# Performance work log

Hardware: AMD Instinct MI355X
Metric: run time of the kernel (lower is better)

Reference implementation:

```python
import jax, jax.numpy as jnp
import numpy as np
from jax import lax

B, CIN, L = 2048, 1024, 30
E, C = 8, 2            # num_experts, num_classes
FC_IN = 256 * 9        # 2304
FIN_IN = C + 512 * L + 256 * (L // 2 + 1)  # 19458


def _maxpool1d(x):
    # MaxPool1d(kernel=2, stride=2, padding=1); pad with -inf like torch
    return lax.reduce_window(x, -jnp.inf, lax.max,
                             (1, 1, 2), (1, 1, 2),
                             [(0, 0), (0, 0), (1, 1)])


def _conv1d(x, w):
    # x: [B,Cin,L], w: [Cout,Cin,3], padding=1
    return lax.conv_general_dilated(x, w, (1,), [(1, 1)],
                                    dimension_numbers=('NCH', 'OIH', 'NCH'))


def setup_inputs() -> dict:
    key = jax.random.key(0)
    ks = jax.random.split(key, 16)
    s = 0.02
    inp = {
        'x': jax.random.normal(ks[0], (B, CIN, L), jnp.float32),
        'expert_idx': jax.random.randint(ks[1], (B,), 0, E),
        'conv1_w': jax.random.normal(ks[2], (512, 1024, 3), jnp.float32) * s,
        'conv1_b': jnp.zeros((512,), jnp.float32),
        'conv2_w': jax.random.normal(ks[3], (256, 512, 3), jnp.float32) * s,
        'conv2_b': jnp.zeros((256,), jnp.float32),
        'fc_w': jax.random.normal(ks[4], (1024, FC_IN), jnp.float32) * s,
        'fc_b': jnp.zeros((1024,), jnp.float32),
        'e_w1': jax.random.normal(ks[5], (E, 512, 1024), jnp.float32) * s,
        'e_b1': jnp.zeros((E, 512), jnp.float32),
        'e_w2': jax.random.normal(ks[6], (E, C, 512), jnp.float32) * s,
        'e_b2': jnp.zeros((E, C), jnp.float32),
        'agg_w': jax.random.normal(ks[7], (C, E * C), jnp.float32) * s,
        'agg_b': jnp.zeros((C,), jnp.float32),
        'fin_w': jax.random.normal(ks[8], (C, FIN_IN), jnp.float32) * s,
        'fin_b': jnp.zeros((C,), jnp.float32),
    }
    return inp


def reference(x, expert_idx, conv1_w, conv1_b, conv2_w, conv2_b, fc_w, fc_b,
              e_w1, e_b1, e_w2, e_b2, agg_w, agg_b, fin_w, fin_b):
    b = x.shape[0]
    # shared feature extractor
    x1 = jax.nn.relu(_conv1d(x, conv1_w) + conv1_b[None, :, None])     # [B,512,30]
    p1 = _maxpool1d(x1)                                                 # [B,512,16]
    x2 = jax.nn.relu(_conv1d(p1, conv2_w) + conv2_b[None, :, None])    # [B,256,16]
    p2 = _maxpool1d(x2)                                                 # [B,256,9]
    sf = jax.nn.relu(p2.reshape(b, -1) @ fc_w.T + fc_b)                 # [B,1024]

    # expert dispatch: run all experts densely, then select per-sample
    h = jax.nn.relu(jnp.einsum('bd,ehd->beh', sf, e_w1) + e_b1)        # [B,E,512]
    all_out = jnp.einsum('beh,ech->bec', h, e_w2) + e_b2               # [B,E,C]
    sel = all_out[jnp.arange(b), expert_idx]                           # [B,C]
    oh = jax.nn.one_hot(expert_idx, E, dtype=sel.dtype)                # [B,E]
    expert_outputs = (oh[:, :, None] * sel[:, None, :]).reshape(b, E * C)

    agg = expert_outputs @ agg_w.T + agg_b                             # [B,C]
    combined = jnp.concatenate(
        [agg, x1.reshape(b, -1), x2.reshape(b, -1)], axis=1)           # [B,19458]
    return combined @ fin_w.T + fin_b                                  # [B,C]
```

## Files before the change

kernel.cpp:

```cpp
#include <hip/hip_runtime.h>
#include <hip/hip_bf16.h>

typedef short short8 __attribute__((ext_vector_type(8)));
typedef short short4v __attribute__((ext_vector_type(4)));
typedef float f32x4 __attribute__((ext_vector_type(4)));

__device__ __forceinline__ float bf2f(short s) {
  return __builtin_bit_cast(float, (unsigned)((unsigned short)s) << 16);
}
__device__ __forceinline__ short f2bf(float f) {
  return __builtin_bit_cast(short, __float2bfloat16(f));
}
__device__ __forceinline__ void g2lds16(const void* g, void* l) {
  __builtin_amdgcn_global_load_lds((const __attribute__((address_space(1))) void*)g,
                                   (__attribute__((address_space(3))) void*)l, 16, 0, 0);
}


__global__ __launch_bounds__(256) void prep_x(const float* __restrict__ x, short* __restrict__ xt) {
  __shared__ float tile[64 * 30];
  const int b = blockIdx.x, ci0 = blockIdx.y * 64, t = threadIdx.x;
  const float* src = x + ((long)b * 1024 + ci0) * 30;
  for (int i = t; i < 480; i += 256)
    ((float4*)tile)[i] = ((const float4*)src)[i];
  __syncthreads();
  short* dst = xt + (long)b * 32 * 1024 + ci0;
  for (int i = t; i < 512; i += 256) {
    int lp = i >> 4, cq = i & 15;
    short4v v = {0, 0, 0, 0};
    if (lp >= 1 && lp <= 30) {
#pragma unroll
      for (int u = 0; u < 4; ++u) v[u] = f2bf(tile[(cq * 4 + u) * 30 + lp - 1]);
    }
    *(short4v*)&dst[(long)lp * 1024 + cq * 4] = v;
  }
}

__global__ __launch_bounds__(256) void prep_weights(
    const float* __restrict__ conv1_w, const float* __restrict__ conv2_w,
    const float* __restrict__ fc_w, const float* __restrict__ e_w1,
    const float* __restrict__ fin_w,
    short* __restrict__ w1t, short* __restrict__ w2t, short* __restrict__ fcwt,
    short* __restrict__ ew1t, float* __restrict__ finw1, float* __restrict__ finw2) {
  const int T0 = 1572864;
  const int T1 = T0 + 393216;
  const int T2 = T1 + 2359296;
  const int T3 = T2 + 4194304;
  const int T4 = T3 + 30720;
  const int T5 = T4 + 8192;
  for (long idx = (long)blockIdx.x * 256 + threadIdx.x; idx < T5;
       idx += (long)gridDim.x * 256) {
    if (idx < T0) {
      int i = (int)idx; int co = i / 3072, j = i % 3072, k = j >> 10, ci = j & 1023;
      w1t[i] = f2bf(conv1_w[(co * 1024 + ci) * 3 + k]);
    } else if (idx < T1) {
      int i = (int)(idx - T0); int co = i / 1536, j = i % 1536, k = j >> 9, ci = j & 511;
      w2t[i] = f2bf(conv2_w[(co * 512 + ci) * 3 + k]);
    } else if (idx < T2) {
      int i = (int)(idx - T1); int n = i / 2304, j = i % 2304, jj = j >> 8, co = j & 255;
      fcwt[i] = f2bf(fc_w[n * 2304 + co * 9 + jj]);
    } else if (idx < T3) {
      int i = (int)(idx - T2);
      ew1t[i] = f2bf(e_w1[i]);
    } else if (idx < T4) {
      int i = (int)(idx - T3); int c = i / 15360, r = i % 15360, l = r >> 9, co = r & 511;
      finw1[i] = fin_w[c * 19458 + 2 + co * 30 + l];
    } else {
      int i = (int)(idx - T4); int c = i / 4096, r = i % 4096, l = r >> 8, co = r & 255;
      finw2[i] = fin_w[c * 19458 + 2 + 15360 + co * 16 + l];
    }
  }
}

__global__ __launch_bounds__(512, 2) void gemm256_bt_relu(
    const short* __restrict__ A, const short* __restrict__ Bm, short* __restrict__ C,
    const float* __restrict__ bias, int N, int K, int L, int S1, int S2, int nNB) {
  __shared__ __align__(16) short lA0[256 * 64], lA1[256 * 64];
  __shared__ __align__(16) short lB0[256 * 64], lB1[256 * 64];
  const int t = threadIdx.x, wave = t >> 6, lane = t & 63;
  const int wr = wave >> 2, wc = wave & 3;
  const int nwg = gridDim.x, qn = nwg >> 3, bid = blockIdx.x;
  const int swz = (bid & 7) * qn + (bid >> 3);
  const int m0 = (swz / nNB) * 256, n0 = (swz % nNB) * 256;
  const int srow = t >> 3;
  const int scol = (((t & 7) ^ (srow & 7)) * 8);

  long aoff[4], boff[4];
#pragma unroll
  for (int q = 0; q < 4; ++q) {
    int m = m0 + q * 64 + srow;
    aoff[q] = (long)(m / L) * S1 + (long)(m % L) * S2 + scol;
    boff[q] = (long)(n0 + q * 64 + srow) * K + scol;
  }
  const int ldst = wave * 512 + lane * 8;

  f32x4 acc[8][4];
#pragma unroll
  for (int i = 0; i < 8; ++i)
#pragma unroll
    for (int j = 0; j < 4; ++j) acc[i][j] = f32x4{0.f, 0.f, 0.f, 0.f};

  const int l7 = lane & 7, g4 = lane >> 4, r16 = lane & 15;
  const int nK = K >> 6;

#define STAGE256(k0, dA, dB) do {                                     \
    const long kk0_ = (long)(k0);                                     \
    _Pragma("unroll")                                                 \
    for (int q = 0; q < 4; ++q) {                                     \
      g2lds16(A + aoff[q] + kk0_, &dA[q * 4096 + ldst]);              \
      g2lds16(Bm + boff[q] + kk0_, &dB[q * 4096 + ldst]);             \
    } } while (0)

#define PHASES256(sA, sB) do {                                                        \
    short8 af[4][2], bfr[4][2];                                                       \
                                 \
    _Pragma("unroll") for (int kk = 0; kk < 2; ++kk) {                                \
      const int jb = ((kk * 4 + g4) ^ l7) * 8;                                        \
      _Pragma("unroll") for (int i = 0; i < 4; ++i)                                   \
        af[i][kk] = *(const short8*)&sA[(wr * 128 + i * 16 + r16) * 64 + jb];         \
      _Pragma("unroll") for (int j = 0; j < 2; ++j)                                   \
        bfr[j][kk] = *(const short8*)&sB[(wc * 64 + j * 16 + r16) * 64 + jb];         \
    }                                                                                 \
    __builtin_amdgcn_s_setprio(1);                                                    \
    _Pragma("unroll") for (int i = 0; i < 4; ++i)                                     \
    _Pragma("unroll") for (int j = 0; j < 2; ++j)                                     \
    _Pragma("unroll") for (int kk = 0; kk < 2; ++kk)                                  \
      acc[i][j] = __builtin_amdgcn_mfma_f32_16x16x32_bf16(af[i][kk], bfr[j][kk], acc[i][j], 0, 0, 0); \
    __builtin_amdgcn_s_setprio(0);                                                    \
                                         \
    _Pragma("unroll") for (int kk = 0; kk < 2; ++kk) {                                \
      const int jb = ((kk * 4 + g4) ^ l7) * 8;                                        \
      _Pragma("unroll") for (int j = 0; j < 2; ++j)                                   \
        bfr[2 + j][kk] = *(const short8*)&sB[(wc * 64 + (2 + j) * 16 + r16) * 64 + jb]; \
    }                                                                                 \
    __builtin_amdgcn_s_setprio(1);                                                    \
    _Pragma("unroll") for (int i = 0; i < 4; ++i)                                     \
    _Pragma("unroll") for (int j = 0; j < 2; ++j)                                     \
    _Pragma("unroll") for (int kk = 0; kk < 2; ++kk)                                  \
      acc[i][2 + j] = __builtin_amdgcn_mfma_f32_16x16x32_bf16(af[i][kk], bfr[2 + j][kk], acc[i][2 + j], 0, 0, 0); \
    __builtin_amdgcn_s_setprio(0);                                                    \
                                         \
    _Pragma("unroll") for (int kk = 0; kk < 2; ++kk) {                                \
      const int jb = ((kk * 4 + g4) ^ l7) * 8;                                        \
      _Pragma("unroll") for (int i = 0; i < 4; ++i)                                   \
        af[i][kk] = *(const short8*)&sA[(wr * 128 + (4 + i) * 16 + r16) * 64 + jb];   \
    }                                                                                 \
    __builtin_amdgcn_s_setprio(1);                                                    \
    _Pragma("unroll") for (int i = 0; i < 4; ++i)                                     \
    _Pragma("unroll") for (int j = 0; j < 2; ++j)                                     \
    _Pragma("unroll") for (int kk = 0; kk < 2; ++kk)                                  \
      acc[4 + i][2 + j] = __builtin_amdgcn_mfma_f32_16x16x32_bf16(af[i][kk], bfr[2 + j][kk], acc[4 + i][2 + j], 0, 0, 0); \
    __builtin_amdgcn_s_setprio(0);                                                    \
                                \
    __builtin_amdgcn_s_setprio(1);                                                    \
    _Pragma("unroll") for (int i = 0; i < 4; ++i)                                     \
    _Pragma("unroll") for (int j = 0; j < 2; ++j)                                     \
    _Pragma("unroll") for (int kk = 0; kk < 2; ++kk)                                  \
      acc[4 + i][j] = __builtin_amdgcn_mfma_f32_16x16x32_bf16(af[i][kk], bfr[j][kk], acc[4 + i][j], 0, 0, 0); \
    __builtin_amdgcn_s_setprio(0);                                                    \
  } while (0)

  STAGE256(0, lA0, lB0);
  for (int ktp = 0; ktp < (nK >> 1); ++ktp) {
    const int t1 = 2 * ktp + 1;
    __syncthreads();
    STAGE256((long)t1 << 6, lA1, lB1);
    PHASES256(lA0, lB0);
    __syncthreads();
    if (t1 + 1 < nK) STAGE256((long)(t1 + 1) << 6, lA0, lB0);
    PHASES256(lA1, lB1);
  }

#pragma unroll
  for (int j = 0; j < 4; ++j) {
    int col = n0 + wc * 64 + j * 16 + r16;
    float bv = bias[col];
#pragma unroll
    for (int i = 0; i < 8; ++i) {
      int rbase = m0 + wr * 128 + i * 16 + (g4 << 2);
#pragma unroll
      for (int r = 0; r < 4; ++r) {
        float o = fmaxf(acc[i][j][r] + bv, 0.f);
        C[(long)(rbase + r) * N + col] = f2bf(o);
      }
    }
  }
#undef STAGE256
#undef PHASES256
}

__global__ __launch_bounds__(256, 2) void gemm128_bt_relu(
    const short* __restrict__ A, const short* __restrict__ Bm, short* __restrict__ C,
    const float* __restrict__ bias, int N, int K, int L, int S1, int S2, int nNB) {
  __shared__ __align__(16) short lA0[128 * 64], lA1[128 * 64];
  __shared__ __align__(16) short lB0[128 * 64], lB1[128 * 64];
  const int t = threadIdx.x, wave = t >> 6, lane = t & 63;
  const int wr = wave >> 1, wc = wave & 1;
  const int nwg = gridDim.x, qn = nwg >> 3, bid = blockIdx.x;
  const int swz = (bid & 7) * qn + (bid >> 3);
  const int m0 = (swz / nNB) * 128, n0 = (swz % nNB) * 128;
  const int arow = t >> 3;
  const int acolg = (((t & 7) ^ (arow & 7)) * 8);

  long aoff[4], boff[4];
#pragma unroll
  for (int qq = 0; qq < 4; ++qq) {
    int m = m0 + qq * 32 + arow;
    aoff[qq] = (long)(m / L) * S1 + (long)(m % L) * S2 + acolg;
    boff[qq] = (long)(n0 + qq * 32 + arow) * K + acolg;
  }
  const int ldst = wave * 512 + lane * 8;

  f32x4 acc[4][4];
#pragma unroll
  for (int i = 0; i < 4; ++i)
#pragma unroll
    for (int j = 0; j < 4; ++j) acc[i][j] = f32x4{0.f, 0.f, 0.f, 0.f};

  const int l7 = lane & 7, g4 = lane >> 4, r16 = lane & 15;
  const int nK = K >> 6;

#define STAGE128(k0, dA, dB) do {                                     \
    const long kk0_ = (long)(k0);                                     \
    _Pragma("unroll")                                                 \
    for (int qq = 0; qq < 4; ++qq) {                                  \
      g2lds16(A + aoff[qq] + kk0_, &dA[qq * 2048 + ldst]);            \
      g2lds16(Bm + boff[qq] + kk0_, &dB[qq * 2048 + ldst]);           \
    } } while (0)

#define PHASES128(sA, sB) do {                                                        \
    _Pragma("unroll")                                                                 \
    for (int kk = 0; kk < 2; ++kk) {                                                  \
      const int jblk = ((kk * 4 + g4) ^ l7) * 8;                                      \
      short8 af[4], bfv[4];                                                           \
      _Pragma("unroll") for (int i = 0; i < 4; ++i)                                   \
        af[i] = *(const short8*)&sA[(wr * 64 + i * 16 + r16) * 64 + jblk];            \
      _Pragma("unroll") for (int j = 0; j < 4; ++j)                                   \
        bfv[j] = *(const short8*)&sB[(wc * 64 + j * 16 + r16) * 64 + jblk];           \
      __builtin_amdgcn_s_setprio(1);                                                  \
      _Pragma("unroll") for (int i = 0; i < 4; ++i)                                   \
      _Pragma("unroll") for (int j = 0; j < 4; ++j)                                   \
        acc[i][j] = __builtin_amdgcn_mfma_f32_16x16x32_bf16(af[i], bfv[j], acc[i][j], 0, 0, 0); \
      __builtin_amdgcn_s_setprio(0);                                                  \
    } } while (0)

  STAGE128(0, lA0, lB0);
  for (int ktp = 0; ktp < (nK >> 1); ++ktp) {
    const int t1 = 2 * ktp + 1;
    __syncthreads();
    STAGE128((long)t1 << 6, lA1, lB1);
    PHASES128(lA0, lB0);
    __syncthreads();
    if (t1 + 1 < nK) STAGE128((long)(t1 + 1) << 6, lA0, lB0);
    PHASES128(lA1, lB1);
  }

#pragma unroll
  for (int j = 0; j < 4; ++j) {
    int col = n0 + wc * 64 + j * 16 + r16;
    float bv = bias[col];
#pragma unroll
    for (int i = 0; i < 4; ++i) {
      int rbase = m0 + wr * 64 + i * 16 + (g4 << 2);
#pragma unroll
      for (int r = 0; r < 4; ++r) {
        float o = fmaxf(acc[i][j][r] + bv, 0.f);
        C[(long)(rbase + r) * N + col] = f2bf(o);
      }
    }
  }
#undef STAGE128
#undef PHASES128
}

__global__ __launch_bounds__(256) void pool1_fused(
    const short* __restrict__ x1t, short* __restrict__ p1t,
    const float* __restrict__ finw1, float* __restrict__ fin1p) {
  const int b = blockIdx.x, t = threadIdx.x, lane = t & 63, wave = t >> 6;
  const short* xb = x1t + (long)b * 15360;
  short* pb = p1t + (long)b * 9216;
  for (int i = t; i < 2304; i += 256) {
    int c4 = i & 127, jp = i >> 7;
    short4v v = {0, 0, 0, 0};
    if (jp >= 1 && jp <= 16) {
      int j = jp - 1, l0 = 2 * j - 1, l1 = 2 * j;
      short4v a = (l0 >= 0) ? *(const short4v*)&xb[l0 * 512 + c4 * 4] : short4v{0, 0, 0, 0};
      short4v bb = (l1 < 30) ? *(const short4v*)&xb[l1 * 512 + c4 * 4] : short4v{0, 0, 0, 0};
#pragma unroll
      for (int u = 0; u < 4; ++u) v[u] = f2bf(fmaxf(bf2f(a[u]), bf2f(bb[u])));
    }
    *(short4v*)&pb[i * 4] = v;
  }
  float f0 = 0.f, f1 = 0.f;
#pragma unroll
  for (int it = 0; it < 15; ++it) {
    int i = (it * 256 + t) * 4;
    short4v xv = *(const short4v*)&xb[i];
    float4 w0 = *(const float4*)&finw1[i];
    float4 w1 = *(const float4*)&finw1[15360 + i];
    float a0 = bf2f(xv[0]), a1 = bf2f(xv[1]), a2 = bf2f(xv[2]), a3 = bf2f(xv[3]);
    f0 += a0 * w0.x + a1 * w0.y + a2 * w0.z + a3 * w0.w;
    f1 += a0 * w1.x + a1 * w1.y + a2 * w1.z + a3 * w1.w;
  }
#pragma unroll
  for (int off = 32; off > 0; off >>= 1) {
    f0 += __shfl_down(f0, off);
    f1 += __shfl_down(f1, off);
  }
  __shared__ float red[4][2];
  if (lane == 0) { red[wave][0] = f0; red[wave][1] = f1; }
  __syncthreads();
  if (t == 0) {
    float F0 = red[0][0] + red[1][0] + red[2][0] + red[3][0];
    float F1 = red[0][1] + red[1][1] + red[2][1] + red[3][1];
    fin1p[b * 2 + 0] = F0;
    fin1p[b * 2 + 1] = F1;
  }
}

__global__ __launch_bounds__(256) void pool2_fused(
    const short* __restrict__ x2t, short* __restrict__ p2t,
    const float* __restrict__ finw2, float* __restrict__ fin2p) {
  const int b = blockIdx.x, t = threadIdx.x, lane = t & 63, wave = t >> 6;
  const short* xb = x2t + (long)b * 4096;
  short* pb = p2t + (long)b * 2304;
  for (int i = t; i < 576; i += 256) {
    int c4 = i & 63, j = i >> 6;
    int l0 = 2 * j - 1, l1 = 2 * j;
    short4v a = (l0 >= 0) ? *(const short4v*)&xb[l0 * 256 + c4 * 4] : short4v{0, 0, 0, 0};
    short4v bb = (l1 < 16) ? *(const short4v*)&xb[l1 * 256 + c4 * 4] : short4v{0, 0, 0, 0};
    short4v v;
#pragma unroll
    for (int u = 0; u < 4; ++u) v[u] = f2bf(fmaxf(bf2f(a[u]), bf2f(bb[u])));
    *(short4v*)&pb[i * 4] = v;
  }
  float f0 = 0.f, f1 = 0.f;
#pragma unroll
  for (int it = 0; it < 4; ++it) {
    int i = (it * 256 + t) * 4;
    short4v xv = *(const short4v*)&xb[i];
    float4 w0 = *(const float4*)&finw2[i];
    float4 w1 = *(const float4*)&finw2[4096 + i];
    float a0 = bf2f(xv[0]), a1 = bf2f(xv[1]), a2 = bf2f(xv[2]), a3 = bf2f(xv[3]);
    f0 += a0 * w0.x + a1 * w0.y + a2 * w0.z + a3 * w0.w;
    f1 += a0 * w1.x + a1 * w1.y + a2 * w1.z + a3 * w1.w;
  }
#pragma unroll
  for (int off = 32; off > 0; off >>= 1) {
    f0 += __shfl_down(f0, off);
    f1 += __shfl_down(f1, off);
  }
  __shared__ float red[4][2];
  if (lane == 0) { red[wave][0] = f0; red[wave][1] = f1; }
  __syncthreads();
  if (t == 0) {
    fin2p[b * 2 + 0] = red[0][0] + red[1][0] + red[2][0] + red[3][0];
    fin2p[b * 2 + 1] = red[0][1] + red[1][1] + red[2][1] + red[3][1];
  }
}

__global__ __launch_bounds__(64) void final_k(
    const short* __restrict__ h, const int* __restrict__ eidx,
    const float* __restrict__ e_w2, const float* __restrict__ e_b2,
    const float* __restrict__ agg_w, const float* __restrict__ agg_b,
    const float* __restrict__ fin_w, const float* __restrict__ fin_b,
    const float* __restrict__ fin1p, const float* __restrict__ fin2p,
    float* __restrict__ out) {
  const int b = blockIdx.x, lane = threadIdx.x;
  const int e = eidx[b];
  const short* hp = h + (long)b * 4096 + e * 512;
  const float* w20 = e_w2 + (e * 2 + 0) * 512;
  const float* w21 = e_w2 + (e * 2 + 1) * 512;
  float s0 = 0.f, s1 = 0.f;
#pragma unroll
  for (int it = 0; it < 8; ++it) {
    int i = it * 64 + lane;
    float hv = bf2f(hp[i]);
    s0 += hv * w20[i];
    s1 += hv * w21[i];
  }
#pragma unroll
  for (int off = 32; off > 0; off >>= 1) {
    s0 += __shfl_down(s0, off);
    s1 += __shfl_down(s1, off);
  }
  if (lane == 0) {
    float sel0 = s0 + e_b2[e * 2 + 0];
    float sel1 = s1 + e_b2[e * 2 + 1];
    float agg0 = sel0 * agg_w[e * 2] + sel1 * agg_w[e * 2 + 1] + agg_b[0];
    float agg1 = sel0 * agg_w[16 + e * 2] + sel1 * agg_w[16 + e * 2 + 1] + agg_b[1];
    float F0 = fin1p[b * 2 + 0] + fin2p[b * 2 + 0];
    float F1 = fin1p[b * 2 + 1] + fin2p[b * 2 + 1];
    out[b * 2 + 0] = F0 + agg0 * fin_w[0] + agg1 * fin_w[1] + fin_b[0];
    out[b * 2 + 1] = F1 + agg0 * fin_w[19458 + 0] + agg1 * fin_w[19458 + 1] + fin_b[1];
  }
}

extern "C" void kernel_launch(void* const* d_in, const int* in_sizes, int n_in,
                              void* d_out, int out_size, void* d_ws, size_t ws_size,
                              hipStream_t stream) {
  const float* x       = (const float*)d_in[0];
  const int*   eidx    = (const int*)d_in[1];
  const float* conv1_w = (const float*)d_in[2];
  const float* conv1_b = (const float*)d_in[3];
  const float* conv2_w = (const float*)d_in[4];
  const float* conv2_b = (const float*)d_in[5];
  const float* fc_w    = (const float*)d_in[6];
  const float* fc_b    = (const float*)d_in[7];
  const float* e_w1    = (const float*)d_in[8];
  const float* e_b1    = (const float*)d_in[9];
  const float* e_w2    = (const float*)d_in[10];
  const float* e_b2    = (const float*)d_in[11];
  const float* agg_w   = (const float*)d_in[12];
  const float* agg_b   = (const float*)d_in[13];
  const float* fin_w   = (const float*)d_in[14];
  const float* fin_b   = (const float*)d_in[15];
  float* out = (float*)d_out;

  char* ws = (char*)d_ws;
  short* xt    = (short*)(ws + 0L);
  short* x1t   = (short*)(ws + 134217728L);
  short* p1t   = (short*)(ws + 197132288L);
  short* x2t   = (short*)(ws + 234881024L);
  short* p2t   = (short*)(ws + 251658240L);
  short* sf    = (short*)(ws + 261095424L);
  short* h     = (short*)(ws + 265289728L);
  short* w1t   = (short*)(ws + 282066944L);
  short* w2t   = (short*)(ws + 285212672L);
  short* fcwt  = (short*)(ws + 285999104L);
  short* ew1t  = (short*)(ws + 290717696L);
  float* finw1 = (float*)(ws + 299106304L);
  float* finw2 = (float*)(ws + 299229184L);
  float* fin1p = (float*)(ws + 0L);
  float* fin2p = (float*)(ws + 16384L);

  prep_weights<<<4096, 256, 0, stream>>>(conv1_w, conv2_w, fc_w, e_w1, fin_w,
                                         w1t, w2t, fcwt, ew1t, finw1, finw2);
  prep_x<<<dim3(2048, 16), 256, 0, stream>>>(x, xt);
  gemm256_bt_relu<<<480, 512, 0, stream>>>(xt, w1t, x1t, conv1_b, 512, 3072, 30, 32768, 1024, 2);
  pool1_fused<<<2048, 256, 0, stream>>>(x1t, p1t, finw1, fin1p);
  gemm128_bt_relu<<<512, 256, 0, stream>>>(p1t, w2t, x2t, conv2_b, 256, 1536, 16, 9216, 512, 2);
  pool2_fused<<<2048, 256, 0, stream>>>(x2t, p2t, finw2, fin2p);
  gemm128_bt_relu<<<128, 256, 0, stream>>>(p2t, fcwt, sf, fc_b, 1024, 2304, 1, 2304, 0, 8);
  gemm128_bt_relu<<<512, 256, 0, stream>>>(sf, ew1t, h, e_b1, 4096, 1024, 1, 1024, 0, 32);
  final_k<<<2048, 64, 0, stream>>>(h, eidx, e_w2, e_b2, agg_w, agg_b,
                                   fin_w, fin_b, fin1p, fin2p, out);
}
```

Baseline: 395.7 us.

## Compute only the selected expert's hidden layer via grouped gather GEMM

Replaces the dense all-experts first-layer GEMM (B x 4096 x 1024) with a per-expert grouped GEMM. A single-block kernel builds a list of row indices for each expert, and the GEMM gathers the sf rows for that expert and writes only the selected hidden vectors. This cuts expert FLOPs by roughly the number of experts. The price is a serial row-list kernel (one thread per expert looping over 2048 samples), an extra launch, and some idle blocks when the per-expert counts are uneven.

```diff
diff --git a/kernel.cpp b/kernel.cpp
--- a/kernel.cpp
+++ b/kernel.cpp
@@ -113,7 +113,6 @@
 
 #define PHASES256(sA, sB) do {                                                        \
     short8 af[4][2], bfr[4][2];                                                       \
-                                 \
     _Pragma("unroll") for (int kk = 0; kk < 2; ++kk) {                                \
       const int jb = ((kk * 4 + g4) ^ l7) * 8;                                        \
       _Pragma("unroll") for (int i = 0; i < 4; ++i)                                   \
@@ -127,7 +126,6 @@
     _Pragma("unroll") for (int kk = 0; kk < 2; ++kk)                                  \
       acc[i][j] = __builtin_amdgcn_mfma_f32_16x16x32_bf16(af[i][kk], bfr[j][kk], acc[i][j], 0, 0, 0); \
     __builtin_amdgcn_s_setprio(0);                                                    \
-                                         \
     _Pragma("unroll") for (int kk = 0; kk < 2; ++kk) {                                \
       const int jb = ((kk * 4 + g4) ^ l7) * 8;                                        \
       _Pragma("unroll") for (int j = 0; j < 2; ++j)                                   \
@@ -139,7 +137,6 @@
     _Pragma("unroll") for (int kk = 0; kk < 2; ++kk)                                  \
       acc[i][2 + j] = __builtin_amdgcn_mfma_f32_16x16x32_bf16(af[i][kk], bfr[2 + j][kk], acc[i][2 + j], 0, 0, 0); \
     __builtin_amdgcn_s_setprio(0);                                                    \
-                                         \
     _Pragma("unroll") for (int kk = 0; kk < 2; ++kk) {                                \
       const int jb = ((kk * 4 + g4) ^ l7) * 8;                                        \
       _Pragma("unroll") for (int i = 0; i < 4; ++i)                                   \
@@ -151,7 +148,6 @@
     _Pragma("unroll") for (int kk = 0; kk < 2; ++kk)                                  \
       acc[4 + i][2 + j] = __builtin_amdgcn_mfma_f32_16x16x32_bf16(af[i][kk], bfr[2 + j][kk], acc[4 + i][2 + j], 0, 0, 0); \
     __builtin_amdgcn_s_setprio(0);                                                    \
-                                \
     __builtin_amdgcn_s_setprio(1);                                                    \
     _Pragma("unroll") for (int i = 0; i < 4; ++i)                                     \
     _Pragma("unroll") for (int j = 0; j < 2; ++j)                                     \
@@ -273,6 +269,113 @@
 #undef PHASES128
 }
 
+__global__ __launch_bounds__(64) void build_rowlist(
+    const int* __restrict__ eidx, int* __restrict__ rowl, int* __restrict__ cnt) {
+  const int e = threadIdx.x;
+  if (e >= 8) return;
+  int c = 0;
+  int* dst = rowl + e * 2048;
+  for (int b = 0; b < 2048; ++b)
+    if (eidx[b] == e) dst[c++] = b;
+  cnt[e] = c;
+  int fill = (c > 0) ? dst[0] : 0;
+  int cpad = (c + 127) & ~127;
+  for (int i = c; i < cpad; ++i) dst[i] = fill;
+}
+
+__global__ __launch_bounds__(256, 2) void gemm128_gather_relu(
+    const short* __restrict__ A, const short* __restrict__ ew1t, short* __restrict__ hsel,
+    const float* __restrict__ e_b1, const int* __restrict__ rowl, const int* __restrict__ cnt) {
+  const int bid = blockIdx.x;
+  const int e = bid >> 6, sub = bid & 63;
+  const int mt = sub >> 2, nt = sub & 3;
+  const int ce = cnt[e];
+  const int m0 = mt * 128;
+  if (m0 >= ce) return;
+  const int n0 = nt * 128;
+  const int* rl = rowl + e * 2048;
+  const short* Bm = ew1t + (long)e * 512 * 1024;
+
+  __shared__ __align__(16) short lA0[128 * 64], lA1[128 * 64];
+  __shared__ __align__(16) short lB0[128 * 64], lB1[128 * 64];
+  const int t = threadIdx.x, wave = t >> 6, lane = t & 63;
+  const int wr = wave >> 1, wc = wave & 1;
+  const int arow = t >> 3;
+  const int acolg = (((t & 7) ^ (arow & 7)) * 8);
+
+  long aoff[4], boff[4];
+#pragma unroll
+  for (int qq = 0; qq < 4; ++qq) {
+    aoff[qq] = (long)rl[m0 + qq * 32 + arow] * 1024 + acolg;
+    boff[qq] = (long)(n0 + qq * 32 + arow) * 1024 + acolg;
+  }
+  const int ldst = wave * 512 + lane * 8;
+
+  f32x4 acc[4][4];
+#pragma unroll
+  for (int i = 0; i < 4; ++i)
+#pragma unroll
+    for (int j = 0; j < 4; ++j) acc[i][j] = f32x4{0.f, 0.f, 0.f, 0.f};
+
+  const int l7 = lane & 7, g4 = lane >> 4, r16 = lane & 15;
+  const int nK = 16;
+
+#define STAGEG(k0, dA, dB) do {                                       \
+    const long kk0_ = (long)(k0);                                     \
+    _Pragma("unroll")                                                 \
+    for (int qq = 0; qq < 4; ++qq) {                                  \
+      g2lds16(A + aoff[qq] + kk0_, &dA[qq * 2048 + ldst]);            \
+      g2lds16(Bm + boff[qq] + kk0_, &dB[qq * 2048 + ldst]);           \
+    } } while (0)
+
+#define PHASESG(sA, sB) do {                                                          \
+    _Pragma("unroll")                                                                 \
+    for (int kk = 0; kk < 2; ++kk) {                                                  \
+      const int jblk = ((kk * 4 + g4) ^ l7) * 8;                                      \
+      short8 af[4], bfv[4];                                                           \
+      _Pragma("unroll") for (int i = 0; i < 4; ++i)                                   \
+        af[i] = *(const short8*)&sA[(wr * 64 + i * 16 + r16) * 64 + jblk];            \
+      _Pragma("unroll") for (int j = 0; j < 4; ++j)                                   \
+        bfv[j] = *(const short8*)&sB[(wc * 64 + j * 16 + r16) * 64 + jblk];           \
+      __builtin_amdgcn_s_setprio(1);                                                  \
+      _Pragma("unroll") for (int i = 0; i < 4; ++i)                                   \
+      _Pragma("unroll") for (int j = 0; j < 4; ++j)                                   \
+        acc[i][j] = __builtin_amdgcn_mfma_f32_16x16x32_bf16(af[i], bfv[j], acc[i][j], 0, 0, 0); \
+      __builtin_amdgcn_s_setprio(0);                                                  \
+    } } while (0)
+
+  STAGEG(0, lA0, lB0);
+  for (int ktp = 0; ktp < (nK >> 1); ++ktp) {
+    const int t1 = 2 * ktp + 1;
+    __syncthreads();
+    STAGEG((long)t1 << 6, lA1, lB1);
+    PHASESG(lA0, lB0);
+    __syncthreads();
+    if (t1 + 1 < nK) STAGEG((long)(t1 + 1) << 6, lA0, lB0);
+    PHASESG(lA1, lB1);
+  }
+
+#pragma unroll
+  for (int j = 0; j < 4; ++j) {
+    int col = n0 + wc * 64 + j * 16 + r16;
+    float bv = e_b1[e * 512 + col];
+#pragma unroll
+    for (int i = 0; i < 4; ++i) {
+      int rbase = m0 + wr * 64 + i * 16 + (g4 << 2);
+#pragma unroll
+      for (int r = 0; r < 4; ++r) {
+        int mrow = rbase + r;
+        if (mrow < ce) {
+          float o = fmaxf(acc[i][j][r] + bv, 0.f);
+          hsel[(long)rl[mrow] * 512 + col] = f2bf(o);
+        }
+      }
+    }
+  }
+#undef STAGEG
+#undef PHASESG
+}
+
 __global__ __launch_bounds__(256) void pool1_fused(
     const short* __restrict__ x1t, short* __restrict__ p1t,
     const float* __restrict__ finw1, float* __restrict__ fin1p) {
@@ -311,10 +414,8 @@
   if (lane == 0) { red[wave][0] = f0; red[wave][1] = f1; }
   __syncthreads();
   if (t == 0) {
-    float F0 = red[0][0] + red[1][0] + red[2][0] + red[3][0];
-    float F1 = red[0][1] + red[1][1] + red[2][1] + red[3][1];
-    fin1p[b * 2 + 0] = F0;
-    fin1p[b * 2 + 1] = F1;
+    fin1p[b * 2 + 0] = red[0][0] + red[1][0] + red[2][0] + red[3][0];
+    fin1p[b * 2 + 1] = red[0][1] + red[1][1] + red[2][1] + red[3][1];
   }
 }
 
@@ -360,7 +461,7 @@
 }
 
 __global__ __launch_bounds__(64) void final_k(
-    const short* __restrict__ h, const int* __restrict__ eidx,
+    const short* __restrict__ hsel, const int* __restrict__ eidx,
     const float* __restrict__ e_w2, const float* __restrict__ e_b2,
     const float* __restrict__ agg_w, const float* __restrict__ agg_b,
     const float* __restrict__ fin_w, const float* __restrict__ fin_b,
@@ -368,7 +469,7 @@
     float* __restrict__ out) {
   const int b = blockIdx.x, lane = threadIdx.x;
   const int e = eidx[b];
-  const short* hp = h + (long)b * 4096 + e * 512;
+  const short* hp = hsel + (long)b * 512;
   const float* w20 = e_w2 + (e * 2 + 0) * 512;
   const float* w21 = e_w2 + (e * 2 + 1) * 512;
   float s0 = 0.f, s1 = 0.f;
@@ -433,6 +534,9 @@
   float* finw2 = (float*)(ws + 299229184L);
   float* fin1p = (float*)(ws + 0L);
   float* fin2p = (float*)(ws + 16384L);
+  int*   rowl  = (int*)(ws + 32768L);
+  int*   cntp  = (int*)(ws + 98304L);
+  short* hsel  = (short*)(ws + 131072L);
 
   prep_weights<<<4096, 256, 0, stream>>>(conv1_w, conv2_w, fc_w, e_w1, fin_w,
                                          w1t, w2t, fcwt, ew1t, finw1, finw2);
@@ -442,7 +546,8 @@
   gemm128_bt_relu<<<512, 256, 0, stream>>>(p1t, w2t, x2t, conv2_b, 256, 1536, 16, 9216, 512, 2);
   pool2_fused<<<2048, 256, 0, stream>>>(x2t, p2t, finw2, fin2p);
   gemm128_bt_relu<<<128, 256, 0, stream>>>(p2t, fcwt, sf, fc_b, 1024, 2304, 1, 2304, 0, 8);
-  gemm128_bt_relu<<<512, 256, 0, stream>>>(sf, ew1t, h, e_b1, 4096, 1024, 1, 1024, 0, 32);
-  final_k<<<2048, 64, 0, stream>>>(h, eidx, e_w2, e_b2, agg_w, agg_b,
+  build_rowlist<<<1, 64, 0, stream>>>(eidx, rowl, cntp);
+  gemm128_gather_relu<<<512, 256, 0, stream>>>(sf, ew1t, hsel, e_b1, rowl, cntp);
+  final_k<<<2048, 64, 0, stream>>>(hsel, eidx, e_w2, e_b2, agg_w, agg_b,
                                    fin_w, fin_b, fin1p, fin2p, out);
 }
```

Result: slower. 557.2 us (+40.8%).
